# Kernel tuning notes

Hardware: AMD Instinct MI355X
Metric: run time of the kernel (lower is better)

## Reference

```python
import jax, jax.numpy as jnp
import numpy as np

N_CHANNELS = 512
GROUPS = 8
EPS = 1e-5


def setup_inputs() -> dict:
    key = jax.random.key(0)
    ks = jax.random.split(key, 7)
    B, C, L = 8, N_CHANNELS, 4096
    s = 1.0 / np.sqrt(C)
    return {
        "x": jax.random.normal(ks[0], (B, C, L), dtype=jnp.float32),
        "gamma": jnp.ones((C,), dtype=jnp.float32),
        "beta": jnp.zeros((C,), dtype=jnp.float32),
        "w_qkv": jax.random.normal(ks[1], (3 * C, C), dtype=jnp.float32) * s,
        "b_qkv": jax.random.normal(ks[2], (3 * C,), dtype=jnp.float32) * 0.01,
        "w_out": jax.random.normal(ks[3], (C, C), dtype=jnp.float32) * s,
        "b_out": jax.random.normal(ks[4], (C,), dtype=jnp.float32) * 0.01,
    }


def group_norm(x, gamma, beta):
    # x: [B, C, L]; normalize per group of C//GROUPS channels over (channels_in_group, L)
    B, C, L = x.shape
    xg = x.reshape(B, GROUPS, C // GROUPS, L)
    mean = xg.mean(axis=(2, 3), keepdims=True)
    var = xg.var(axis=(2, 3), keepdims=True)
    xn = ((xg - mean) * jax.lax.rsqrt(var + EPS)).reshape(B, C, L)
    return xn * gamma[None, :, None] + beta[None, :, None]


def reference(x, gamma, beta, w_qkv, b_qkv, w_out, b_out):
    B, C, L = x.shape
    xn = group_norm(x, gamma, beta)
    # 1x1 conv == channel matmul: [3C, C] @ [B, C, L] -> [B, 3C, L]
    qkv = jnp.einsum('oc,bcl->bol', w_qkv, xn) + b_qkv[None, :, None]
    q, k, v = jnp.split(qkv, 3, axis=1)  # each [B, C, L]
    scale = C ** (-0.5)
    attn = jnp.einsum('bcl,bck->blk', q, k) * scale  # [B, L, L]
    attn = jax.nn.softmax(attn, axis=-1)
    out = jnp.einsum('blk,bck->bcl', attn, v)  # [B, C, L]
    proj = jnp.einsum('oc,bcl->bol', w_out, out) + b_out[None, :, None]
    return x + proj
```

## Files before the change

kernel.cpp:

```cpp
#include <hip/hip_runtime.h>

typedef __attribute__((ext_vector_type(4))) float f32x4;
typedef __attribute__((ext_vector_type(8))) short short8;
typedef unsigned short u16;
typedef unsigned int u32;
typedef unsigned char u8;

static constexpr int Bb = 8, Cc = 512, Ll = 4096;

__device__ __forceinline__ u16 f2bf(float f) {
  u32 u = __builtin_bit_cast(u32, f);
  u = (u + 0x7FFFu + ((u >> 16) & 1u)) >> 16;
  return (u16)u;
}

__device__ __forceinline__ u8 f2e4m3(float f) {
  u32 u = __builtin_bit_cast(u32, f);
  u8 s = (u >> 24) & 0x80;
  float af = __builtin_fabsf(f);
  if (af >= 448.f) return s | 0x7E;
  if (af < 0.015625f) {
    int n = (int)rintf(af * 512.f);
    return s | (u8)n;
  }
  u32 b = u & 0x7FFFFFFF;
  u32 r = b + 0x7FFFF + ((b >> 20) & 1);
  int e = (int)(r >> 23) - 127;
  if (e > 8) return s | 0x7E;
  return s | (u8)(((e + 7) << 3) | ((r >> 20) & 7));
}

__device__ __forceinline__ void load_lds16(const void* g, void* l) {
  __builtin_amdgcn_global_load_lds((const __attribute__((address_space(1))) void*)g,
                                   (__attribute__((address_space(3))) void*)l,
                                   16, 0, 0);
}

__global__ void cvt_bf16_kernel(const float* __restrict__ src, u16* __restrict__ dst, int n) {
  int stride = gridDim.x * blockDim.x;
  for (int i = blockIdx.x * blockDim.x + threadIdx.x; i < n; i += stride)
    dst[i] = f2bf(src[i]);
}

__global__ __launch_bounds__(256)
void gn_stats_kernel(const float* __restrict__ x, float* __restrict__ stats) {
  int bg = blockIdx.x;
  const f32x4* p = (const f32x4*)(x + (size_t)bg * (64 * Ll));
  float s = 0.f, ss = 0.f;
  for (int i = threadIdx.x; i < 64 * Ll / 4; i += 256) {
    f32x4 v = p[i];
    s  += v[0] + v[1] + v[2] + v[3];
    ss += v[0]*v[0] + v[1]*v[1] + v[2]*v[2] + v[3]*v[3];
  }
  __shared__ float rs[256], rq[256];
  rs[threadIdx.x] = s; rq[threadIdx.x] = ss;
  __syncthreads();
  for (int st = 128; st > 0; st >>= 1) {
    if (threadIdx.x < st) { rs[threadIdx.x] += rs[threadIdx.x + st]; rq[threadIdx.x] += rq[threadIdx.x + st]; }
    __syncthreads();
  }
  if (threadIdx.x == 0) {
    const float inv_n = 1.f / (64.f * 4096.f);
    float mean = rs[0] * inv_n;
    float var  = rq[0] * inv_n - mean * mean;
    stats[bg * 2]     = mean;
    stats[bg * 2 + 1] = rsqrtf(var + 1e-5f);
  }
}

__global__ __launch_bounds__(256)
void gn_apply_t_kernel(const float* __restrict__ x, const float* __restrict__ gamma,
                       const float* __restrict__ beta, const float* __restrict__ stats,
                       u16* __restrict__ xn_t) {
  int lt = blockIdx.x;
  int ct = blockIdx.y;
  int b  = blockIdx.z;
  __shared__ float tile[64][65];
  int t = threadIdx.x;
  int lx = t & 63;
  int qd = t >> 6;
  int c0 = ct * 64, l0 = lt * 64;
  float mean = stats[(b * 8 + ct) * 2];
  float rstd = stats[(b * 8 + ct) * 2 + 1];
  #pragma unroll
  for (int i = 0; i < 16; ++i) {
    int cl = qd + i * 4;
    int c = c0 + cl;
    float v = x[((size_t)b * Cc + c) * Ll + l0 + lx];
    tile[cl][lx] = (v - mean) * rstd * gamma[c] + beta[c];
  }
  __syncthreads();
  #pragma unroll
  for (int i = 0; i < 16; ++i) {
    int ll = qd + i * 4;
    xn_t[((size_t)b * Ll + l0 + ll) * Cc + c0 + lx] = f2bf(tile[lx][ll]);
  }
}

template <int MODE>
__global__ __launch_bounds__(256, 2)
void gemm_tn(const u16* __restrict__ A, long long aStride, int lda,
             const u16* __restrict__ Bm, long long bStride, int ldb,
             void* __restrict__ Dv, long long dStride, int ldd,
             const float* __restrict__ bias, const float* __restrict__ resid, int K) {
  int z = blockIdx.z;
  A  += (size_t)z * aStride;
  Bm += (size_t)z * bStride;
  int m0 = blockIdx.x * 128, n0 = blockIdx.y * 128;
  __shared__ uint4 sA[1024], sB[1024];
  int tid = threadIdx.x, lane = tid & 63;
  int wv = tid >> 6, wr = wv >> 1, wc = wv & 1;
  int l15 = lane & 15, l4 = lane >> 4;
  f32x4 acc[4][4] = {};
  for (int kt = 0; kt < K; kt += 64) {
    __syncthreads();
    #pragma unroll
    for (int p = 0; p < 4; ++p) {
      int s = p * 256 + tid;
      int r = ((s >> 7) << 4) | (((s >> 2) & 1) << 3) | ((s >> 3) & 7);
      int g = (((s >> 6) & 1) << 2) | (s & 3);
      load_lds16(A  + (size_t)(m0 + r) * lda + kt + g * 8, &sA[s]);
      load_lds16(Bm + (size_t)(n0 + r) * ldb + kt + g * 8, &sB[s]);
    }
    __syncthreads();
    #pragma unroll
    for (int ks = 0; ks < 2; ++ks) {
      short8 af[4], bfr[4];
      #pragma unroll
      for (int i = 0; i < 4; ++i) {
        int sa = (4 * wr + i) * 128 + ks * 64 + (l15 & 7) * 8 + (l15 >> 3) * 4 + l4;
        af[i]  = *(const short8*)&sA[sa];
        int sb = (4 * wc + i) * 128 + ks * 64 + (l15 & 7) * 8 + (l15 >> 3) * 4 + l4;
        bfr[i] = *(const short8*)&sB[sb];
      }
      #pragma unroll
      for (int i = 0; i < 4; ++i)
        #pragma unroll
        for (int j = 0; j < 4; ++j)
          acc[i][j] = __builtin_amdgcn_mfma_f32_16x16x32_bf16(af[i], bfr[j], acc[i][j], 0, 0, 0);
    }
  }
  #pragma unroll
  for (int i = 0; i < 4; ++i) {
    #pragma unroll
    for (int j = 0; j < 4; ++j) {
      #pragma unroll
      for (int r = 0; r < 4; ++r) {
        int m = m0 + 64 * wr + 16 * i + 4 * l4 + r;
        int n = n0 + 64 * wc + 16 * j + l15;
        float val = acc[i][j][r] + ((MODE == 0 || MODE == 3) ? bias[n] : bias[m]);
        if (MODE == 3) {
          u8* base = (n < 512) ? (u8*)Dv : (u8*)const_cast<float*>(resid);
          base[(size_t)z * dStride + (size_t)m * ldd + (n & 511)] = f2e4m3(val);
        } else {
          size_t idx = (size_t)z * dStride + (size_t)m * ldd + n;
          if (MODE == 2)      ((float*)Dv)[idx] = val + resid[idx];
          else                ((u16*)Dv)[idx]   = f2bf(val);
        }
      }
    }
  }
}

__global__ __launch_bounds__(512, 2)
void flash_attn_kernel(const u8* __restrict__ q8, const u8* __restrict__ k8,
                       const u16* __restrict__ v, u16* __restrict__ o_t) {
  int bid = blockIdx.x;
  int b  = bid & 7;
  int q0 = (bid >> 3) * 128;
  int tid = threadIdx.x, lane = tid & 63, wv = tid >> 6;
  int l15 = lane & 15, l4 = lane >> 4;
  const u8* q8b = q8 + (size_t)b * Ll * 512;
  const u8* k8b = k8 + (size_t)b * Ll * 512;
  const u16* vb = v   + (size_t)b * Cc * Ll;
  u16* ob       = o_t + (size_t)b * Ll * Cc;

  __shared__ uint4 sK[2][1024];
  __shared__ uint4 sV[2][512 * 4];
  __shared__ __align__(16) char sP[128 * 80];
  __shared__ __align__(16) float sAl[128];

  int ow_q = wv >> 2, ow_c = wv & 3;

  long aq[16];
  {
    const u8* qp = q8b + (size_t)(q0 + wv * 16 + l15) * 512 + 8 * l4;
    #pragma unroll
    for (int ks = 0; ks < 16; ++ks) aq[ks] = *(const long*)(qp + 32 * ks);
  }

  auto issueK = [&](int kt, int buf) {
    #pragma unroll
    for (int p = 0; p < 2; ++p) {
      int s = p * 512 + tid;
      int r = s >> 5, g = s & 31;
      load_lds16(k8b + (size_t)(kt * 32 + r) * 512 + ((g ^ (r & 15)) << 4), &sK[buf][s]);
    }
  };
  auto issueV = [&](int kt, int buf) {
    #pragma unroll
    for (int p = 0; p < 4; ++p) {
      int s = p * 512 + tid;
      int r = s >> 2, g = s & 3, gw = g ^ ((r >> 1) & 3);
      load_lds16(vb + (size_t)r * Ll + kt * 32 + gw * 8, &sV[buf][s]);
    }
  };
  issueK(0, 0);
  issueV(0, 0);

  f32x4 accO[4][8];
  #pragma unroll
  for (int i = 0; i < 4; ++i)
    #pragma unroll
    for (int j = 0; j < 8; ++j) accO[i][j] = (f32x4){0.f, 0.f, 0.f, 0.f};
  float mrun = -1e30f, lrun = 0.f;
  const float scale = 0.044194173824159216f;

  const int NT = Ll / 32;
  for (int kt = 0; kt < NT; ++kt) {
    int buf = kt & 1;
    __syncthreads();
    if (kt + 1 < NT) { issueK(kt + 1, buf ^ 1); issueV(kt + 1, buf ^ 1); }

    const u8* kb = (const u8*)&sK[buf][0];
    f32x4 s2[2];
    #pragma unroll
    for (int t = 0; t < 2; ++t) {
      s2[t] = (f32x4){0.f, 0.f, 0.f, 0.f};
      int row = 16 * t + l15;
      #pragma unroll
      for (int ks = 0; ks < 16; ++ks) {
        int gr = (2 * ks + (l4 >> 1)) ^ (row & 15);
        long ak = *(const long*)(kb + row * 512 + (gr << 4) + 8 * (l4 & 1));
        s2[t] = __builtin_amdgcn_mfma_f32_16x16x32_fp8_fp8(ak, aq[ks], s2[t], 0, 0, 0);
      }
    }

    #pragma unroll
    for (int t = 0; t < 2; ++t)
      #pragma unroll
      for (int r = 0; r < 4; ++r) s2[t][r] *= scale;
    float mx = fmaxf(fmaxf(s2[0][0], s2[0][1]), fmaxf(s2[0][2], s2[0][3]));
    mx = fmaxf(mx, fmaxf(fmaxf(s2[1][0], s2[1][1]), fmaxf(s2[1][2], s2[1][3])));
    mx = fmaxf(mx, __shfl_xor(mx, 16));
    mx = fmaxf(mx, __shfl_xor(mx, 32));
    float mnew = fmaxf(mrun, mx);
    float al = __expf(mrun - mnew);
    mrun = mnew;
    float ps = 0.f;
    #pragma unroll
    for (int t = 0; t < 2; ++t)
      #pragma unroll
      for (int r = 0; r < 4; ++r) { float pv = __expf(s2[t][r] - mnew); s2[t][r] = pv; ps += pv; }
    ps += __shfl_xor(ps, 16);
    ps += __shfl_xor(ps, 32);
    lrun = lrun * al + ps;

    {
      char* pb = sP + (16 * wv + l15) * 80;
      #pragma unroll
      for (int t = 0; t < 2; ++t) {
        u32 lo = (u32)f2bf(s2[t][0]) | ((u32)f2bf(s2[t][1]) << 16);
        u32 hi = (u32)f2bf(s2[t][2]) | ((u32)f2bf(s2[t][3]) << 16);
        uint2 w = {lo, hi};
        *(uint2*)(pb + 32 * t + 8 * l4) = w;
      }
      if (lane < 16) sAl[16 * wv + lane] = al;
    }

    __builtin_amdgcn_sched_barrier(0);
    asm volatile("s_waitcnt lgkmcnt(0)" ::: "memory");
    __builtin_amdgcn_s_barrier();
    __builtin_amdgcn_sched_barrier(0);

    #pragma unroll
    for (int i = 0; i < 4; ++i) {
      f32x4 av = *(const f32x4*)&sAl[64 * ow_q + 16 * i + 4 * l4];
      #pragma unroll
      for (int j = 0; j < 8; ++j) {
        #pragma unroll
        for (int r = 0; r < 4; ++r) accO[i][j][r] *= av[r];
      }
    }
    short8 ap[4];
    #pragma unroll
    for (int i = 0; i < 4; ++i) {
      int ra = 64 * ow_q + 16 * i + l15;
      ap[i] = *(const short8*)(sP + ra * 80 + 16 * l4);
    }
    const uint4* vbuf = &sV[buf][0];
    #pragma unroll
    for (int j = 0; j < 8; ++j) {
      int crow = 128 * ow_c + 16 * j + l15;
      short8 bv = *(const short8*)&vbuf[crow * 4 + (l4 ^ ((crow >> 1) & 3))];
      #pragma unroll
      for (int i = 0; i < 4; ++i)
        accO[i][j] = __builtin_amdgcn_mfma_f32_16x16x32_bf16(ap[i], bv, accO[i][j], 0, 0, 0);
    }
  }

  __syncthreads();
  if (lane < 16) sAl[16 * wv + lane] = lrun;
  __syncthreads();
  #pragma unroll
  for (int i = 0; i < 4; ++i) {
    f32x4 lv = *(const f32x4*)&sAl[64 * ow_q + 16 * i + 4 * l4];
    #pragma unroll
    for (int r = 0; r < 4; ++r) lv[r] = 1.f / lv[r];
    #pragma unroll
    for (int j = 0; j < 8; ++j) {
      #pragma unroll
      for (int r = 0; r < 4; ++r) {
        int q = q0 + 64 * ow_q + 16 * i + 4 * l4 + r;
        int c = 128 * ow_c + 16 * j + l15;
        ob[(size_t)q * Cc + c] = f2bf(accO[i][j][r] * lv[r]);
      }
    }
  }
}

extern "C" void kernel_launch(void* const* d_in, const int* in_sizes, int n_in,
                              void* d_out, int out_size, void* d_ws, size_t ws_size,
                              hipStream_t stream) {
  const float* x     = (const float*)d_in[0];
  const float* gamma = (const float*)d_in[1];
  const float* beta  = (const float*)d_in[2];
  const float* w_qkv = (const float*)d_in[3];
  const float* b_qkv = (const float*)d_in[4];
  const float* w_out = (const float*)d_in[5];
  const float* b_out = (const float*)d_in[6];
  float* out = (float*)d_out;

  char* ws = (char*)d_ws;
  size_t off = 0;
  auto alloc = [&](size_t bytes) -> char* {
    char* p = ws + off;
    off += (bytes + 1023) & ~(size_t)1023;
    return p;
  };
  float* stats = (float*)alloc(64 * 2 * sizeof(float));
  u16* wqb = (u16*)alloc((size_t)1536 * 512 * 2);
  u16* wob = (u16*)alloc((size_t)512 * 512 * 2);
  u16* xnt = (u16*)alloc((size_t)Bb * Ll * Cc * 2);
  u8*  q8  = (u8*)alloc((size_t)Bb * Ll * 512);
  u8*  k8  = (u8*)alloc((size_t)Bb * Ll * 512);
  u16* vbf = (u16*)alloc((size_t)Bb * Cc * Ll * 2);
  u16* ot  = xnt;
  if (off > ws_size) return;

  cvt_bf16_kernel<<<256, 256, 0, stream>>>(w_qkv, wqb, 1536 * 512);
  cvt_bf16_kernel<<<256, 256, 0, stream>>>(w_out, wob, 512 * 512);
  gn_stats_kernel<<<64, 256, 0, stream>>>(x, stats);
  gn_apply_t_kernel<<<dim3(64, 8, 8), 256, 0, stream>>>(x, gamma, beta, stats, xnt);
  gemm_tn<3><<<dim3(32, 8, 8), 256, 0, stream>>>(
      xnt, (long long)Ll * Cc, Cc, wqb, 0, Cc,
      q8, (long long)Ll * 512, 512, b_qkv, (const float*)k8, Cc);
  gemm_tn<1><<<dim3(4, 32, 8), 256, 0, stream>>>(
      wqb + (size_t)1024 * 512, 0, Cc, xnt, (long long)Ll * Cc, Cc,
      vbf, (long long)Cc * Ll, Ll, b_qkv + 1024, nullptr, Cc);
  flash_attn_kernel<<<256, 512, 0, stream>>>(q8, k8, vbf, ot);
  gemm_tn<2><<<dim3(4, 32, 8), 256, 0, stream>>>(
      wob, 0, Cc, ot, (long long)Ll * Cc, Cc,
      out, (long long)Cc * Ll, Ll, b_out, x, Cc);
}
```

Before: 642.5 us.

## Use FP8 for V and softmax probabilities in the attention PV matmul

The V projection GEMM now writes V as FP8 e4m3 instead of bf16. The attention kernel converts the probabilities P to FP8 with a fast custom rounding, offset by a fixed 2^6 so they use the FP8 range better, and computes P·V with the fp8 MFMA. The softmax moves to exp2 with a log2-scaled softmax scale. This halves V global traffic and LDS footprint and doubles the PV MFMA rate, at the cost of lower precision in P and V.

```diff
diff --git a/kernel.cpp b/kernel.cpp
--- a/kernel.cpp
+++ b/kernel.cpp
@@ -28,6 +28,13 @@
   int e = (int)(r >> 23) - 127;
   if (e > 8) return s | 0x7E;
   return s | (u8)(((e + 7) << 3) | ((r >> 20) & 7));
+}
+
+__device__ __forceinline__ u32 p2fp8(float f) {
+  u32 u = __builtin_bit_cast(u32, f);
+  u32 r = u + 0x7FFFFu + ((u >> 20) & 1u);
+  u32 v = ((r >> 20) - (120u << 3)) & 0x7Fu;
+  return r >= 0x3C800000u ? v : 0u;
 }
 
 __device__ __forceinline__ void load_lds16(const void* g, void* l) {
@@ -152,6 +159,8 @@
         if (MODE == 3) {
           u8* base = (n < 512) ? (u8*)Dv : (u8*)const_cast<float*>(resid);
           base[(size_t)z * dStride + (size_t)m * ldd + (n & 511)] = f2e4m3(val);
+        } else if (MODE == 4) {
+          ((u8*)Dv)[(size_t)z * dStride + (size_t)m * ldd + n] = f2e4m3(val);
         } else {
           size_t idx = (size_t)z * dStride + (size_t)m * ldd + n;
           if (MODE == 2)      ((float*)Dv)[idx] = val + resid[idx];
@@ -164,7 +173,7 @@
 
 __global__ __launch_bounds__(512, 2)
 void flash_attn_kernel(const u8* __restrict__ q8, const u8* __restrict__ k8,
-                       const u16* __restrict__ v, u16* __restrict__ o_t) {
+                       const u8* __restrict__ v8, u16* __restrict__ o_t) {
   int bid = blockIdx.x;
   int b  = bid & 7;
   int q0 = (bid >> 3) * 128;
@@ -172,12 +181,12 @@
   int l15 = lane & 15, l4 = lane >> 4;
   const u8* q8b = q8 + (size_t)b * Ll * 512;
   const u8* k8b = k8 + (size_t)b * Ll * 512;
-  const u16* vb = v   + (size_t)b * Cc * Ll;
+  const u8* vb8 = v8 + (size_t)b * Cc * Ll;
   u16* ob       = o_t + (size_t)b * Ll * Cc;
 
   __shared__ uint4 sK[2][1024];
-  __shared__ uint4 sV[2][512 * 4];
-  __shared__ __align__(16) char sP[128 * 80];
+  __shared__ uint4 sV[2][1024];
+  __shared__ __align__(16) char sP[128 * 48];
   __shared__ __align__(16) float sAl[128];
 
   int ow_q = wv >> 2, ow_c = wv & 3;
@@ -199,10 +208,10 @@
   };
   auto issueV = [&](int kt, int buf) {
     #pragma unroll
-    for (int p = 0; p < 4; ++p) {
+    for (int p = 0; p < 2; ++p) {
       int s = p * 512 + tid;
-      int r = s >> 2, g = s & 3, gw = g ^ ((r >> 1) & 3);
-      load_lds16(vb + (size_t)r * Ll + kt * 32 + gw * 8, &sV[buf][s]);
+      int r = s >> 1, g = s & 1;
+      load_lds16(vb8 + (size_t)r * Ll + kt * 32 + 16 * (g ^ ((r >> 2) & 1)), &sV[buf][s]);
     }
   };
   issueK(0, 0);
@@ -214,7 +223,7 @@
     #pragma unroll
     for (int j = 0; j < 8; ++j) accO[i][j] = (f32x4){0.f, 0.f, 0.f, 0.f};
   float mrun = -1e30f, lrun = 0.f;
-  const float scale = 0.044194173824159216f;
+  const float scale_l2 = 0.06375871784902f;
 
   const int NT = Ll / 32;
   for (int kt = 0; kt < NT; ++kt) {
@@ -239,31 +248,31 @@
     #pragma unroll
     for (int t = 0; t < 2; ++t)
       #pragma unroll
-      for (int r = 0; r < 4; ++r) s2[t][r] *= scale;
+      for (int r = 0; r < 4; ++r) s2[t][r] *= scale_l2;
     float mx = fmaxf(fmaxf(s2[0][0], s2[0][1]), fmaxf(s2[0][2], s2[0][3]));
     mx = fmaxf(mx, fmaxf(fmaxf(s2[1][0], s2[1][1]), fmaxf(s2[1][2], s2[1][3])));
     mx = fmaxf(mx, __shfl_xor(mx, 16));
     mx = fmaxf(mx, __shfl_xor(mx, 32));
     float mnew = fmaxf(mrun, mx);
-    float al = __expf(mrun - mnew);
+    float al = exp2f(mrun - mnew);
     mrun = mnew;
+    float mb = mnew - 6.f;
     float ps = 0.f;
     #pragma unroll
     for (int t = 0; t < 2; ++t)
       #pragma unroll
-      for (int r = 0; r < 4; ++r) { float pv = __expf(s2[t][r] - mnew); s2[t][r] = pv; ps += pv; }
+      for (int r = 0; r < 4; ++r) { float pv = exp2f(s2[t][r] - mb); s2[t][r] = pv; ps += pv; }
     ps += __shfl_xor(ps, 16);
     ps += __shfl_xor(ps, 32);
     lrun = lrun * al + ps;
 
     {
-      char* pb = sP + (16 * wv + l15) * 80;
+      char* pb = sP + (16 * wv + l15) * 48;
       #pragma unroll
       for (int t = 0; t < 2; ++t) {
-        u32 lo = (u32)f2bf(s2[t][0]) | ((u32)f2bf(s2[t][1]) << 16);
-        u32 hi = (u32)f2bf(s2[t][2]) | ((u32)f2bf(s2[t][3]) << 16);
-        uint2 w = {lo, hi};
-        *(uint2*)(pb + 32 * t + 8 * l4) = w;
+        u32 w = p2fp8(s2[t][0]) | (p2fp8(s2[t][1]) << 8) |
+                (p2fp8(s2[t][2]) << 16) | (p2fp8(s2[t][3]) << 24);
+        *(u32*)(pb + 16 * t + 4 * l4) = w;
       }
       if (lane < 16) sAl[16 * wv + lane] = al;
     }
@@ -282,20 +291,20 @@
         for (int r = 0; r < 4; ++r) accO[i][j][r] *= av[r];
       }
     }
-    short8 ap[4];
+    long ap[4];
     #pragma unroll
     for (int i = 0; i < 4; ++i) {
       int ra = 64 * ow_q + 16 * i + l15;
-      ap[i] = *(const short8*)(sP + ra * 80 + 16 * l4);
-    }
-    const uint4* vbuf = &sV[buf][0];
+      ap[i] = *(const long*)(sP + ra * 48 + 8 * l4);
+    }
+    const u8* vbuf = (const u8*)&sV[buf][0];
     #pragma unroll
     for (int j = 0; j < 8; ++j) {
       int crow = 128 * ow_c + 16 * j + l15;
-      short8 bv = *(const short8*)&vbuf[crow * 4 + (l4 ^ ((crow >> 1) & 3))];
+      long bv = *(const long*)(vbuf + crow * 32 + ((8 * l4) ^ (((crow >> 2) & 1) << 4)));
       #pragma unroll
       for (int i = 0; i < 4; ++i)
-        accO[i][j] = __builtin_amdgcn_mfma_f32_16x16x32_bf16(ap[i], bv, accO[i][j], 0, 0, 0);
+        accO[i][j] = __builtin_amdgcn_mfma_f32_16x16x32_fp8_fp8(ap[i], bv, accO[i][j], 0, 0, 0);
     }
   }
 
@@ -344,7 +353,7 @@
   u16* xnt = (u16*)alloc((size_t)Bb * Ll * Cc * 2);
   u8*  q8  = (u8*)alloc((size_t)Bb * Ll * 512);
   u8*  k8  = (u8*)alloc((size_t)Bb * Ll * 512);
-  u16* vbf = (u16*)alloc((size_t)Bb * Cc * Ll * 2);
+  u8*  v8  = (u8*)alloc((size_t)Bb * Cc * Ll);
   u16* ot  = xnt;
   if (off > ws_size) return;
 
@@ -355,10 +364,10 @@
   gemm_tn<3><<<dim3(32, 8, 8), 256, 0, stream>>>(
       xnt, (long long)Ll * Cc, Cc, wqb, 0, Cc,
       q8, (long long)Ll * 512, 512, b_qkv, (const float*)k8, Cc);
-  gemm_tn<1><<<dim3(4, 32, 8), 256, 0, stream>>>(
+  gemm_tn<4><<<dim3(4, 32, 8), 256, 0, stream>>>(
       wqb + (size_t)1024 * 512, 0, Cc, xnt, (long long)Ll * Cc, Cc,
-      vbf, (long long)Cc * Ll, Ll, b_qkv + 1024, nullptr, Cc);
-  flash_attn_kernel<<<256, 512, 0, stream>>>(q8, k8, vbf, ot);
+      v8, (long long)Cc * Ll, Ll, b_qkv + 1024, nullptr, Cc);
+  flash_attn_kernel<<<256, 512, 0, stream>>>(q8, k8, v8, ot);
   gemm_tn<2><<<dim3(4, 32, 8), 256, 0, stream>>>(
       wob, 0, Cc, ot, (long long)Ll * Cc, Cc,
       out, (long long)Cc * Ll, Ll, b_out, x, Cc);
```

New measurement: 674.3 us. +4.9%, slower.
